# Kernel optimization log

Hardware: AMD Instinct MI355X
Metric: run time of the kernel (lower is better)

The kernel has to match this reference:

```python
import jax, jax.numpy as jnp
import numpy as np

# Dimensions
B_, L_, D_ = 2, 1024, 1024
EXPAND, N_STATE, K_CONV = 2, 16, 4
D_INNER = D_ * EXPAND          # 2048
DT_RANK = (D_ + 15) // 16      # 64 (mamba default: ceil(d_model/16))


def setup_inputs() -> dict:
    key = jax.random.key(0)
    ks = jax.random.split(key, 10)
    sc = 0.02
    x = jax.random.normal(ks[0], (B_, L_, D_), jnp.float32)
    ln_w = jnp.ones((D_,), jnp.float32)
    ln_b = jnp.zeros((D_,), jnp.float32)
    W_in = jax.random.normal(ks[1], (2 * D_INNER, D_), jnp.float32) * sc
    W_conv = jax.random.normal(ks[2], (D_INNER, K_CONV), jnp.float32) * 0.2
    b_conv = jnp.zeros((D_INNER,), jnp.float32)
    W_xproj = jax.random.normal(ks[3], (DT_RANK + 2 * N_STATE, D_INNER), jnp.float32) * sc
    W_dt = jax.random.normal(ks[4], (D_INNER, DT_RANK), jnp.float32) * (DT_RANK ** -0.5)
    # dt bias: inverse softplus of dt ~ U[1e-3, 1e-1] (mamba init)
    dt = jnp.exp(jax.random.uniform(ks[5], (D_INNER,), jnp.float32)
                 * (np.log(0.1) - np.log(0.001)) + np.log(0.001))
    b_dt = dt + jnp.log(-jnp.expm1(-dt))
    # A_log init: log(1..N) per channel (S4D-real init)
    A_log = jnp.log(jnp.broadcast_to(jnp.arange(1, N_STATE + 1, dtype=jnp.float32),
                                     (D_INNER, N_STATE)))
    D_skip = jnp.ones((D_INNER,), jnp.float32)
    W_out = jax.random.normal(ks[6], (D_, D_INNER), jnp.float32) * sc
    return {"x": x, "ln_w": ln_w, "ln_b": ln_b, "W_in": W_in, "W_conv": W_conv,
            "b_conv": b_conv, "W_xproj": W_xproj, "W_dt": W_dt, "b_dt": b_dt,
            "A_log": A_log, "D_skip": D_skip, "W_out": W_out}


def _layernorm(x, w, b, eps=1e-5):
    mu = jnp.mean(x, axis=-1, keepdims=True)
    var = jnp.mean(jnp.square(x - mu), axis=-1, keepdims=True)
    return (x - mu) * jax.lax.rsqrt(var + eps) * w + b


def reference(x, ln_w, ln_b, W_in, W_conv, b_conv, W_xproj, W_dt, b_dt,
              A_log, D_skip, W_out):
    B, L, D = x.shape
    residual = x
    xn = _layernorm(x, ln_w, ln_b)

    # in_proj -> (x_ssm, z), each (B, L, d_inner)
    xz = jnp.einsum('bld,ed->ble', xn, W_in)
    xs, z = jnp.split(xz, 2, axis=-1)

    # causal depthwise conv1d along L + SiLU
    xp = jnp.pad(xs, ((0, 0), (K_CONV - 1, 0), (0, 0)))
    xc = b_conv + sum(xp[:, k:k + L, :] * W_conv[:, k] for k in range(K_CONV))
    xc = jax.nn.silu(xc)

    # input-dependent dt, B, C
    dbl = jnp.einsum('ble,re->blr', xc, W_xproj)
    dt_low = dbl[..., :DT_RANK]
    B_ssm = dbl[..., DT_RANK:DT_RANK + N_STATE]        # (B, L, N)
    C_ssm = dbl[..., DT_RANK + N_STATE:]               # (B, L, N)
    delta = jax.nn.softplus(jnp.einsum('blr,er->ble', dt_low, W_dt) + b_dt)  # (B, L, d_inner)

    A = -jnp.exp(A_log)                                # (d_inner, N)
    dA = jnp.exp(delta[..., None] * A)                 # (B, L, d_inner, N)
    dBx = delta[..., None] * B_ssm[:, :, None, :] * xc[..., None]  # (B, L, d_inner, N)

    def step(h, inp):
        dA_t, dBx_t, C_t = inp
        h = dA_t * h + dBx_t                           # (B, d_inner, N)
        y_t = jnp.einsum('bdn,bn->bd', h, C_t)
        return h, y_t

    h0 = jnp.zeros((B, D_INNER, N_STATE), x.dtype)
    _, ys = jax.lax.scan(step, h0,
                         (dA.transpose(1, 0, 2, 3), dBx.transpose(1, 0, 2, 3),
                          C_ssm.transpose(1, 0, 2)))
    y = ys.transpose(1, 0, 2) + D_skip * xc            # (B, L, d_inner)
    y = y * jax.nn.silu(z)
    out = jnp.einsum('ble,de->bld', y, W_out)
    # dropout is identity in eval mode
    return out + residual
```

## Files before the change

kernel.cpp:

```cpp
#include <hip/hip_runtime.h>
#include <math.h>

#define B_ 2
#define L_ 1024
#define D_ 1024
#define D_INNER 2048
#define DT_RANK 64
#define N_STATE 16
#define NC 32
#define LC 32

typedef __attribute__((ext_vector_type(8))) short bf16x8;
typedef __attribute__((ext_vector_type(4))) float f32x4;

__device__ __forceinline__ unsigned short f2bf(float f) {
  unsigned int u = __float_as_uint(f);
  u += 0x7fffu + ((u >> 16) & 1u);
  return (unsigned short)(u >> 16);
}
__device__ __forceinline__ float bf2f(unsigned short s) {
  return __uint_as_float((unsigned int)s << 16);
}
__device__ __forceinline__ float softplus_f(float v) {
  return (v > 20.0f) ? v : log1pf(__expf(v));
}

__global__ __launch_bounds__(256) void ln_kernel(const float* __restrict__ x,
                                                 const float* __restrict__ w,
                                                 const float* __restrict__ b,
                                                 unsigned short* __restrict__ out) {
  int row = blockIdx.x;
  int tid = threadIdx.x;
  const float* xr = x + (size_t)row * D_;
  float4 v = ((const float4*)xr)[tid];
  float s  = v.x + v.y + v.z + v.w;
  float s2 = v.x*v.x + v.y*v.y + v.z*v.z + v.w*v.w;
  #pragma unroll
  for (int off = 32; off > 0; off >>= 1) {
    s  += __shfl_down(s, off);
    s2 += __shfl_down(s2, off);
  }
  __shared__ float ss[4], ss2[4];
  int wid = tid >> 6, lane = tid & 63;
  if (lane == 0) { ss[wid] = s; ss2[wid] = s2; }
  __syncthreads();
  if (tid == 0) {
    float a  = ss[0] + ss[1] + ss[2] + ss[3];
    float a2 = ss2[0] + ss2[1] + ss2[2] + ss2[3];
    ss[0]  = a  * (1.0f / D_);
    ss2[0] = a2 * (1.0f / D_);
  }
  __syncthreads();
  float mu = ss[0];
  float var = ss2[0] - mu * mu;
  float rstd = rsqrtf(var + 1e-5f);
  float4 wv = ((const float4*)w)[tid];
  float4 bv = ((const float4*)b)[tid];
  ushort4 o;
  o.x = f2bf((v.x - mu) * rstd * wv.x + bv.x);
  o.y = f2bf((v.y - mu) * rstd * wv.y + bv.y);
  o.z = f2bf((v.z - mu) * rstd * wv.z + bv.z);
  o.w = f2bf((v.w - mu) * rstd * wv.w + bv.w);
  ((ushort4*)(out + (size_t)row * D_))[tid] = o;
}

__global__ __launch_bounds__(256) void cvt_bf16_kernel(const float* __restrict__ in,
                                                       unsigned short* __restrict__ out,
                                                       int n4) {
  int i = blockIdx.x * 256 + threadIdx.x;
  if (i >= n4) return;
  float4 v = ((const float4*)in)[i];
  ushort4 o; o.x = f2bf(v.x); o.y = f2bf(v.y); o.z = f2bf(v.z); o.w = f2bf(v.w);
  ((ushort4*)out)[i] = o;
}

__global__ __launch_bounds__(256) void cvt_wxp_kernel(const float* __restrict__ in,
                                                      unsigned short* __restrict__ out) {
  int i = blockIdx.x * 256 + threadIdx.x;
  int row = (i * 4) >> 11;
  ushort4 o = make_ushort4(0, 0, 0, 0);
  if (row < 96) {
    float4 v = ((const float4*)in)[i];
    o.x = f2bf(v.x); o.y = f2bf(v.y); o.z = f2bf(v.z); o.w = f2bf(v.w);
  }
  ((ushort4*)out)[i] = o;
}

template<int EPI, int BMT>
__global__ __launch_bounds__(256) void gemm_mfma(const unsigned short* __restrict__ A, int lda,
                                                 const unsigned short* __restrict__ B, int ldb,
                                                 float* __restrict__ Cf,
                                                 unsigned short* __restrict__ Cb,
                                                 int ldc, int Nguard, int K,
                                                 const float* __restrict__ ep0,
                                                 size_t zstride = 0) {
  __shared__ unsigned short As[BMT * 64];
  __shared__ unsigned short Bs[128 * 64];
  const int tid = threadIdx.x;
  const int lane = tid & 63;
  const int w = tid >> 6;
  const int wr = w >> 1, wc = w & 1;
  const int bm = blockIdx.y * BMT;
  const int bn = blockIdx.x * 128;
  const int l16 = lane & 15;
  constexpr int MW = BMT / 32;

  int kbeg = 0, kend = K;
  if (EPI == 4) {
    int ks = K >> 4;
    kbeg = blockIdx.z * ks;
    kend = kbeg + ks;
    Cf += (size_t)blockIdx.z * zstride;
  }

  f32x4 acc[MW][4];
  #pragma unroll
  for (int m = 0; m < MW; ++m)
    #pragma unroll
    for (int n = 0; n < 4; ++n) acc[m][n] = (f32x4){0.f, 0.f, 0.f, 0.f};

  for (int k0 = kbeg; k0 < kend; k0 += 64) {
    #pragma unroll
    for (int i = 0; i < BMT / 32; ++i) {
      int p = (i * 256 + tid) * 16;
      int r = p >> 7;
      int s = (p >> 4) & 7;
      int cb = ((s ^ (r & 7)) << 3);
      const unsigned short* ga = A + (size_t)(bm + r) * lda + k0 + cb;
      __builtin_amdgcn_global_load_lds(
          (const __attribute__((address_space(1))) void*)ga,
          (__attribute__((address_space(3))) void*)(As + (p >> 1)), 16, 0, 0);
    }
    #pragma unroll
    for (int i = 0; i < 4; ++i) {
      int p = (i * 256 + tid) * 16;
      int r = p >> 7;
      int s = (p >> 4) & 7;
      int cb = ((s ^ (r & 7)) << 3);
      const unsigned short* gb = B + (size_t)(bn + r) * ldb + k0 + cb;
      __builtin_amdgcn_global_load_lds(
          (const __attribute__((address_space(1))) void*)gb,
          (__attribute__((address_space(3))) void*)(Bs + (p >> 1)), 16, 0, 0);
    }
    __syncthreads();
    #pragma unroll
    for (int ks = 0; ks < 2; ++ks) {
      const int slot = ks * 4 + (lane >> 4);
      bf16x8 af[MW], bfr[4];
      #pragma unroll
      for (int m = 0; m < MW; ++m) {
        int ar = wr * (BMT / 2) + m * 16 + l16;
        af[m] = *(const bf16x8*)(As + ar * 64 + ((slot ^ (ar & 7)) << 3));
      }
      #pragma unroll
      for (int n = 0; n < 4; ++n) {
        int br = wc * 64 + n * 16 + l16;
        bfr[n] = *(const bf16x8*)(Bs + br * 64 + ((slot ^ (br & 7)) << 3));
      }
      #pragma unroll
      for (int m = 0; m < MW; ++m)
        #pragma unroll
        for (int n = 0; n < 4; ++n)
          acc[m][n] = __builtin_amdgcn_mfma_f32_16x16x32_bf16(af[m], bfr[n], acc[m][n], 0, 0, 0);
    }
    __syncthreads();
  }

  const int crow0 = bm + wr * (BMT / 2) + (lane >> 4) * 4;
  const int ccol0 = bn + wc * 64 + l16;
  #pragma unroll
  for (int m = 0; m < MW; ++m) {
    #pragma unroll
    for (int n = 0; n < 4; ++n) {
      int c = ccol0 + n * 16;
      if (c >= Nguard) continue;
      #pragma unroll
      for (int r = 0; r < 4; ++r) {
        int rr = crow0 + m * 16 + r;
        float v = acc[m][n][r];
        if (EPI == 2) {
          Cf[(size_t)rr * ldc + c] = v + ep0[(size_t)rr * ldc + c];
        } else if (EPI == 3) {
          if (c < D_INNER) Cf[(size_t)rr * D_INNER + c] = v;
          else             Cb[(size_t)rr * D_INNER + (c - D_INNER)] = f2bf(v);
        } else if (EPI == 5) {
          Cf[(size_t)rr * ldc + c] = softplus_f(v + ep0[c]);
        } else {
          Cf[(size_t)rr * ldc + c] = v;
        }
      }
    }
  }
}

__global__ __launch_bounds__(256) void reduce_dbl_kernel(const float* __restrict__ part,
                                                         float* __restrict__ dblb,
                                                         unsigned short* __restrict__ dtlow_b) {
  int i = blockIdx.x * 256 + threadIdx.x;
  float4 a = ((const float4*)part)[i];
  #pragma unroll
  for (int s = 1; s < 16; ++s) {
    float4 b = ((const float4*)part)[s * 49152 + i];
    a.x += b.x; a.y += b.y; a.z += b.z; a.w += b.w;
  }
  ((float4*)dblb)[i] = a;
  int flat = i * 4;
  int row = flat / 96;
  int col = flat - row * 96;
  if (col < 64) {
    ushort4 o; o.x = f2bf(a.x); o.y = f2bf(a.y); o.z = f2bf(a.z); o.w = f2bf(a.w);
    *(ushort4*)(dtlow_b + (size_t)row * 64 + col) = o;
  }
}

__global__ __launch_bounds__(256) void conv_silu_kernel(const float* __restrict__ xs,
                                                        const float* __restrict__ Wc,
                                                        const float* __restrict__ bc,
                                                        float* __restrict__ xc,
                                                        unsigned short* __restrict__ xcb) {
  int idx = blockIdx.x * 256 + threadIdx.x;
  int e = idx & (D_INNER - 1);
  int t = (idx >> 11) & (L_ - 1);
  float acc = bc[e];
  float w0 = Wc[e * 4 + 0], w1 = Wc[e * 4 + 1], w2 = Wc[e * 4 + 2], w3 = Wc[e * 4 + 3];
  const float* base = xs + (size_t)idx;
  if (t >= 3) acc = fmaf(base[-3 * D_INNER], w0, acc);
  if (t >= 2) acc = fmaf(base[-2 * D_INNER], w1, acc);
  if (t >= 1) acc = fmaf(base[-1 * D_INNER], w2, acc);
  acc = fmaf(base[0], w3, acc);
  float s = acc / (1.0f + __expf(-acc));
  xc[idx] = s;
  xcb[idx] = f2bf(s);
}

__global__ __launch_bounds__(256) void scan1_kernel(const float* __restrict__ delta,
                                                    const float* __restrict__ xc,
                                                    const float* __restrict__ dbl,
                                                    const float* __restrict__ A_log,
                                                    float* __restrict__ P,
                                                    float* __restrict__ Q) {
  int e = blockIdx.x * 256 + threadIdx.x;
  int b = blockIdx.y, c = blockIdx.z;
  const int t0 = (int)(b * L_ + c * LC);

  __shared__ float sB[LC][N_STATE];
  for (int i = threadIdx.x; i < LC * N_STATE; i += 256) {
    int step = i >> 4, n = i & 15;
    sB[step][n] = dbl[(size_t)(t0 + step) * 96 + 64 + n];
  }
  __syncthreads();

  float An[N_STATE];
  #pragma unroll
  for (int q = 0; q < 4; ++q) {
    float4 v = *(const float4*)&A_log[(size_t)e * N_STATE + q * 4];
    An[q*4+0] = -__expf(v.x); An[q*4+1] = -__expf(v.y);
    An[q*4+2] = -__expf(v.z); An[q*4+3] = -__expf(v.w);
  }
  float h[N_STATE], p[N_STATE];
  #pragma unroll
  for (int n = 0; n < N_STATE; ++n) { h[n] = 0.f; p[n] = 1.f; }

  const size_t row0 = (size_t)t0 * D_INNER + e;
  float dlt = delta[row0];
  float xcv = xc[row0];

  for (int tt = 0; tt < LC; ++tt) {
    float ndlt = 0.f, nxcv = 0.f;
    if (tt + 1 < LC) {
      ndlt = delta[row0 + (size_t)(tt + 1) * D_INNER];
      nxcv = xc[row0 + (size_t)(tt + 1) * D_INNER];
    }
    float dbx = dlt * xcv;
    #pragma unroll
    for (int n = 0; n < N_STATE; ++n) {
      float da = __expf(dlt * An[n]);
      h[n] = fmaf(da, h[n], dbx * sB[tt][n]);
      p[n] *= da;
    }
    dlt = ndlt; xcv = nxcv;
  }
  size_t o = ((size_t)(c * B_ + b) * N_STATE) * D_INNER + e;
  #pragma unroll
  for (int n = 0; n < N_STATE; ++n) {
    P[o + (size_t)n * D_INNER] = p[n];
    Q[o + (size_t)n * D_INNER] = h[n];
  }
}

__global__ __launch_bounds__(256) void scan2_kernel(const float* __restrict__ P,
                                                    float* __restrict__ Q) {
  int idx = blockIdx.x * 256 + threadIdx.x;
  float H = 0.f;
  #pragma unroll
  for (int c = 0; c < NC; ++c) {
    size_t o = (size_t)c * (B_ * N_STATE * D_INNER) + idx;
    float p = P[o], q = Q[o];
    Q[o] = H;
    H = fmaf(p, H, q);
  }
}

__global__ __launch_bounds__(256) void scan3_kernel(const float* __restrict__ delta,
                                                    const float* __restrict__ xc,
                                                    const float* __restrict__ dbl,
                                                    const float* __restrict__ A_log,
                                                    const float* __restrict__ Hinit,
                                                    const unsigned short* __restrict__ zb,
                                                    const float* __restrict__ Dsk,
                                                    unsigned short* __restrict__ y) {
  int e = blockIdx.x * 256 + threadIdx.x;
  int b = blockIdx.y, c = blockIdx.z;
  const int t0 = (int)(b * L_ + c * LC);

  __shared__ float sB[LC][N_STATE];
  __shared__ float sC[LC][N_STATE];
  for (int i = threadIdx.x; i < LC * N_STATE; i += 256) {
    int step = i >> 4, n = i & 15;
    const float* row = dbl + (size_t)(t0 + step) * 96;
    sB[step][n] = row[64 + n];
    sC[step][n] = row[80 + n];
  }
  __syncthreads();

  float An[N_STATE];
  #pragma unroll
  for (int q = 0; q < 4; ++q) {
    float4 v = *(const float4*)&A_log[(size_t)e * N_STATE + q * 4];
    An[q*4+0] = -__expf(v.x); An[q*4+1] = -__expf(v.y);
    An[q*4+2] = -__expf(v.z); An[q*4+3] = -__expf(v.w);
  }
  float h[N_STATE];
  {
    size_t o = (size_t)c * (B_ * N_STATE * D_INNER) + (size_t)b * (N_STATE * D_INNER) + e;
    #pragma unroll
    for (int n = 0; n < N_STATE; ++n) h[n] = Hinit[o + (size_t)n * D_INNER];
  }
  float dskip = Dsk[e];
  const size_t row0 = (size_t)t0 * D_INNER + e;

  float dlt = delta[row0];
  float xcv = xc[row0];
  float zv  = bf2f(zb[row0]);

  for (int tt = 0; tt < LC; ++tt) {
    float ndlt = 0.f, nxcv = 0.f, nzv = 0.f;
    if (tt + 1 < LC) {
      ndlt = delta[row0 + (size_t)(tt + 1) * D_INNER];
      nxcv = xc[row0 + (size_t)(tt + 1) * D_INNER];
      nzv  = bf2f(zb[row0 + (size_t)(tt + 1) * D_INNER]);
    }
    float dbx = dlt * xcv;
    float yv = 0.f;
    #pragma unroll
    for (int n = 0; n < N_STATE; ++n) {
      float da = __expf(dlt * An[n]);
      h[n] = fmaf(da, h[n], dbx * sB[tt][n]);
      yv = fmaf(h[n], sC[tt][n], yv);
    }
    float gate = zv / (1.0f + __expf(-zv));
    y[row0 + (size_t)tt * D_INNER] = f2bf((yv + dskip * xcv) * gate);
    dlt = ndlt; xcv = nxcv; zv = nzv;
  }
}

extern "C" void kernel_launch(void* const* d_in, const int* in_sizes, int n_in,
                              void* d_out, int out_size, void* d_ws, size_t ws_size,
                              hipStream_t stream) {
  const float* x       = (const float*)d_in[0];
  const float* ln_w    = (const float*)d_in[1];
  const float* ln_b    = (const float*)d_in[2];
  const float* W_in    = (const float*)d_in[3];
  const float* W_conv  = (const float*)d_in[4];
  const float* b_conv  = (const float*)d_in[5];
  const float* W_xproj = (const float*)d_in[6];
  const float* W_dt    = (const float*)d_in[7];
  const float* b_dt    = (const float*)d_in[8];
  const float* A_log   = (const float*)d_in[9];
  const float* D_skip  = (const float*)d_in[10];
  const float* W_out   = (const float*)d_in[11];
  float* out = (float*)d_out;
  float* ws  = (float*)d_ws;

  const size_t BL = (size_t)B_ * L_;
  float* xs    = ws;
  float* xc    = xs    + BL * D_INNER;
  float* delta = xc    + BL * D_INNER;
  float* dblb  = delta + BL * D_INNER;
  unsigned short* xn_b   = (unsigned short*)(dblb + BL * 96);
  unsigned short* Win_b  = xn_b   + 2097152;
  unsigned short* z_b    = Win_b  + 4194304;
  unsigned short* xc_b   = z_b    + 4194304;
  unsigned short* Wxp_b  = xc_b   + 4194304;
  unsigned short* y_b    = Wxp_b  + 262144;
  unsigned short* Wout_b = y_b    + 4194304;
  unsigned short* dtlow_b= Wout_b + 2097152;
  unsigned short* Wdt_b  = dtlow_b+ 131072;
  float* P    = (float*)xn_b;
  float* Q    = (float*)xc_b;
  float* part = (float*)y_b;

  ln_kernel<<<BL, 256, 0, stream>>>(x, ln_w, ln_b, xn_b);
  cvt_bf16_kernel<<<4096, 256, 0, stream>>>(W_in, Win_b, 1048576);
  cvt_wxp_kernel<<<256, 256, 0, stream>>>(W_xproj, Wxp_b);
  cvt_bf16_kernel<<<128, 256, 0, stream>>>(W_dt, Wdt_b, 32768);
  gemm_mfma<3, 128><<<dim3(32, 16), 256, 0, stream>>>(
      xn_b, D_, Win_b, D_, xs, z_b, D_INNER, 4096, D_, nullptr, 0);
  conv_silu_kernel<<<(BL * D_INNER) / 256, 256, 0, stream>>>(xs, W_conv, b_conv, xc, xc_b);
  gemm_mfma<4, 128><<<dim3(1, 16, 16), 256, 0, stream>>>(
      xc_b, D_INNER, Wxp_b, D_INNER, part, nullptr, 96, 96, D_INNER, nullptr,
      (size_t)2048 * 96);
  reduce_dbl_kernel<<<192, 256, 0, stream>>>(part, dblb, dtlow_b);
  cvt_bf16_kernel<<<2048, 256, 0, stream>>>(W_out, Wout_b, 524288);
  gemm_mfma<5, 128><<<dim3(16, 16), 256, 0, stream>>>(
      dtlow_b, DT_RANK, Wdt_b, DT_RANK, delta, nullptr, D_INNER, D_INNER, DT_RANK, b_dt, 0);
  scan1_kernel<<<dim3(D_INNER / 256, B_, NC), 256, 0, stream>>>(delta, xc, dblb, A_log, P, Q);
  scan2_kernel<<<(B_ * N_STATE * D_INNER) / 256, 256, 0, stream>>>(P, Q);
  scan3_kernel<<<dim3(D_INNER / 256, B_, NC), 256, 0, stream>>>(delta, xc, dblb, A_log, Q,
                                                                z_b, D_skip, y_b);
  gemm_mfma<2, 64><<<dim3(8, 32), 256, 0, stream>>>(
      y_b, D_INNER, Wout_b, D_INNER, out, nullptr, D_, D_, D_INNER, x, 0);
}
```

Measured before the change: 267.4 us.

## Store intermediates in bf16, merge weight conversions, and halve scan chunk length

Stores the in_proj output, delta and the conv output only in bf16, which drops the fp32 copies of xs, xc and delta and cuts memory traffic in the conv and scan kernels. The three weight-conversion kernels become one launch. The scan chunk length changes from 32 to 16, with twice as many chunks, for more parallelism in scan1 and scan3. Workspace now holds separate P and Q buffers. The cost is lower precision in delta and xc during the scan, plus a larger scan2 combine stage.

Result: faster. 260.2 us (-2.7%).

```diff
diff --git a/kernel.cpp b/kernel.cpp
--- a/kernel.cpp
+++ b/kernel.cpp
@@ -7,8 +7,8 @@
 #define D_INNER 2048
 #define DT_RANK 64
 #define N_STATE 16
-#define NC 32
-#define LC 32
+#define NC 64
+#define LC 16
 
 typedef __attribute__((ext_vector_type(8))) short bf16x8;
 typedef __attribute__((ext_vector_type(4))) float f32x4;
@@ -64,26 +64,49 @@
   ((ushort4*)(out + (size_t)row * D_))[tid] = o;
 }
 
-__global__ __launch_bounds__(256) void cvt_bf16_kernel(const float* __restrict__ in,
-                                                       unsigned short* __restrict__ out,
-                                                       int n4) {
+#define N4_WIN  1048576
+#define N4_WOUT  524288
+#define N4_WDT    32768
+#define N4_WXP    65536
+__global__ __launch_bounds__(256) void cvt_all_kernel(const float* __restrict__ W_in,
+                                                      const float* __restrict__ W_out,
+                                                      const float* __restrict__ W_dt,
+                                                      const float* __restrict__ W_xp,
+                                                      unsigned short* __restrict__ Win_b,
+                                                      unsigned short* __restrict__ Wout_b,
+                                                      unsigned short* __restrict__ Wdt_b,
+                                                      unsigned short* __restrict__ Wxp_b) {
   int i = blockIdx.x * 256 + threadIdx.x;
-  if (i >= n4) return;
-  float4 v = ((const float4*)in)[i];
-  ushort4 o; o.x = f2bf(v.x); o.y = f2bf(v.y); o.z = f2bf(v.z); o.w = f2bf(v.w);
-  ((ushort4*)out)[i] = o;
-}
-
-__global__ __launch_bounds__(256) void cvt_wxp_kernel(const float* __restrict__ in,
-                                                      unsigned short* __restrict__ out) {
-  int i = blockIdx.x * 256 + threadIdx.x;
-  int row = (i * 4) >> 11;
-  ushort4 o = make_ushort4(0, 0, 0, 0);
-  if (row < 96) {
-    float4 v = ((const float4*)in)[i];
-    o.x = f2bf(v.x); o.y = f2bf(v.y); o.z = f2bf(v.z); o.w = f2bf(v.w);
-  }
-  ((ushort4*)out)[i] = o;
+  if (i < N4_WIN) {
+    float4 v = ((const float4*)W_in)[i];
+    ushort4 o; o.x = f2bf(v.x); o.y = f2bf(v.y); o.z = f2bf(v.z); o.w = f2bf(v.w);
+    ((ushort4*)Win_b)[i] = o;
+    return;
+  }
+  i -= N4_WIN;
+  if (i < N4_WOUT) {
+    float4 v = ((const float4*)W_out)[i];
+    ushort4 o; o.x = f2bf(v.x); o.y = f2bf(v.y); o.z = f2bf(v.z); o.w = f2bf(v.w);
+    ((ushort4*)Wout_b)[i] = o;
+    return;
+  }
+  i -= N4_WOUT;
+  if (i < N4_WDT) {
+    float4 v = ((const float4*)W_dt)[i];
+    ushort4 o; o.x = f2bf(v.x); o.y = f2bf(v.y); o.z = f2bf(v.z); o.w = f2bf(v.w);
+    ((ushort4*)Wdt_b)[i] = o;
+    return;
+  }
+  i -= N4_WDT;
+  if (i < N4_WXP) {
+    int row = (i * 4) >> 11;
+    ushort4 o = make_ushort4(0, 0, 0, 0);
+    if (row < 96) {
+      float4 v = ((const float4*)W_xp)[i];
+      o.x = f2bf(v.x); o.y = f2bf(v.y); o.z = f2bf(v.z); o.w = f2bf(v.w);
+    }
+    ((ushort4*)Wxp_b)[i] = o;
+  }
 }
 
 template<int EPI, int BMT>
@@ -178,13 +201,12 @@
       for (int r = 0; r < 4; ++r) {
         int rr = crow0 + m * 16 + r;
         float v = acc[m][n][r];
-        if (EPI == 2) {
+        if (EPI == 1) {
+          Cb[(size_t)rr * ldc + c] = f2bf(v);
+        } else if (EPI == 2) {
           Cf[(size_t)rr * ldc + c] = v + ep0[(size_t)rr * ldc + c];
-        } else if (EPI == 3) {
-          if (c < D_INNER) Cf[(size_t)rr * D_INNER + c] = v;
-          else             Cb[(size_t)rr * D_INNER + (c - D_INNER)] = f2bf(v);
         } else if (EPI == 5) {
-          Cf[(size_t)rr * ldc + c] = softplus_f(v + ep0[c]);
+          Cb[(size_t)rr * ldc + c] = f2bf(softplus_f(v + ep0[c]));
         } else {
           Cf[(size_t)rr * ldc + c] = v;
         }
@@ -213,28 +235,27 @@
   }
 }
 
-__global__ __launch_bounds__(256) void conv_silu_kernel(const float* __restrict__ xs,
+__global__ __launch_bounds__(256) void conv_silu_kernel(const unsigned short* __restrict__ xz,
                                                         const float* __restrict__ Wc,
                                                         const float* __restrict__ bc,
-                                                        float* __restrict__ xc,
                                                         unsigned short* __restrict__ xcb) {
   int idx = blockIdx.x * 256 + threadIdx.x;
   int e = idx & (D_INNER - 1);
   int t = (idx >> 11) & (L_ - 1);
+  int bt = idx >> 11;
   float acc = bc[e];
   float w0 = Wc[e * 4 + 0], w1 = Wc[e * 4 + 1], w2 = Wc[e * 4 + 2], w3 = Wc[e * 4 + 3];
-  const float* base = xs + (size_t)idx;
-  if (t >= 3) acc = fmaf(base[-3 * D_INNER], w0, acc);
-  if (t >= 2) acc = fmaf(base[-2 * D_INNER], w1, acc);
-  if (t >= 1) acc = fmaf(base[-1 * D_INNER], w2, acc);
-  acc = fmaf(base[0], w3, acc);
+  const unsigned short* base = xz + (size_t)bt * 4096 + e;
+  if (t >= 3) acc = fmaf(bf2f(base[-3 * 4096]), w0, acc);
+  if (t >= 2) acc = fmaf(bf2f(base[-2 * 4096]), w1, acc);
+  if (t >= 1) acc = fmaf(bf2f(base[-1 * 4096]), w2, acc);
+  acc = fmaf(bf2f(base[0]), w3, acc);
   float s = acc / (1.0f + __expf(-acc));
-  xc[idx] = s;
   xcb[idx] = f2bf(s);
 }
 
-__global__ __launch_bounds__(256) void scan1_kernel(const float* __restrict__ delta,
-                                                    const float* __restrict__ xc,
+__global__ __launch_bounds__(256) void scan1_kernel(const unsigned short* __restrict__ delta,
+                                                    const unsigned short* __restrict__ xc,
                                                     const float* __restrict__ dbl,
                                                     const float* __restrict__ A_log,
                                                     float* __restrict__ P,
@@ -244,8 +265,8 @@
   const int t0 = (int)(b * L_ + c * LC);
 
   __shared__ float sB[LC][N_STATE];
-  for (int i = threadIdx.x; i < LC * N_STATE; i += 256) {
-    int step = i >> 4, n = i & 15;
+  {
+    int step = threadIdx.x >> 4, n = threadIdx.x & 15;
     sB[step][n] = dbl[(size_t)(t0 + step) * 96 + 64 + n];
   }
   __syncthreads();
@@ -262,14 +283,14 @@
   for (int n = 0; n < N_STATE; ++n) { h[n] = 0.f; p[n] = 1.f; }
 
   const size_t row0 = (size_t)t0 * D_INNER + e;
-  float dlt = delta[row0];
-  float xcv = xc[row0];
+  float dlt = bf2f(delta[row0]);
+  float xcv = bf2f(xc[row0]);
 
   for (int tt = 0; tt < LC; ++tt) {
     float ndlt = 0.f, nxcv = 0.f;
     if (tt + 1 < LC) {
-      ndlt = delta[row0 + (size_t)(tt + 1) * D_INNER];
-      nxcv = xc[row0 + (size_t)(tt + 1) * D_INNER];
+      ndlt = bf2f(delta[row0 + (size_t)(tt + 1) * D_INNER]);
+      nxcv = bf2f(xc[row0 + (size_t)(tt + 1) * D_INNER]);
     }
     float dbx = dlt * xcv;
     #pragma unroll
@@ -301,12 +322,12 @@
   }
 }
 
-__global__ __launch_bounds__(256) void scan3_kernel(const float* __restrict__ delta,
-                                                    const float* __restrict__ xc,
+__global__ __launch_bounds__(256) void scan3_kernel(const unsigned short* __restrict__ delta,
+                                                    const unsigned short* __restrict__ xc,
                                                     const float* __restrict__ dbl,
                                                     const float* __restrict__ A_log,
                                                     const float* __restrict__ Hinit,
-                                                    const unsigned short* __restrict__ zb,
+                                                    const unsigned short* __restrict__ xz,
                                                     const float* __restrict__ Dsk,
                                                     unsigned short* __restrict__ y) {
   int e = blockIdx.x * 256 + threadIdx.x;
@@ -315,8 +336,8 @@
 
   __shared__ float sB[LC][N_STATE];
   __shared__ float sC[LC][N_STATE];
-  for (int i = threadIdx.x; i < LC * N_STATE; i += 256) {
-    int step = i >> 4, n = i & 15;
+  {
+    int step = threadIdx.x >> 4, n = threadIdx.x & 15;
     const float* row = dbl + (size_t)(t0 + step) * 96;
     sB[step][n] = row[64 + n];
     sC[step][n] = row[80 + n];
@@ -332,23 +353,24 @@
   }
   float h[N_STATE];
   {
-    size_t o = (size_t)c * (B_ * N_STATE * D_INNER) + (size_t)b * (N_STATE * D_INNER) + e;
+    size_t o = ((size_t)(c * B_ + b) * N_STATE) * D_INNER + e;
     #pragma unroll
     for (int n = 0; n < N_STATE; ++n) h[n] = Hinit[o + (size_t)n * D_INNER];
   }
   float dskip = Dsk[e];
   const size_t row0 = (size_t)t0 * D_INNER + e;
-
-  float dlt = delta[row0];
-  float xcv = xc[row0];
-  float zv  = bf2f(zb[row0]);
+  const size_t zrow0 = (size_t)t0 * 4096 + D_INNER + e;
+
+  float dlt = bf2f(delta[row0]);
+  float xcv = bf2f(xc[row0]);
+  float zv  = bf2f(xz[zrow0]);
 
   for (int tt = 0; tt < LC; ++tt) {
     float ndlt = 0.f, nxcv = 0.f, nzv = 0.f;
     if (tt + 1 < LC) {
-      ndlt = delta[row0 + (size_t)(tt + 1) * D_INNER];
-      nxcv = xc[row0 + (size_t)(tt + 1) * D_INNER];
-      nzv  = bf2f(zb[row0 + (size_t)(tt + 1) * D_INNER]);
+      ndlt = bf2f(delta[row0 + (size_t)(tt + 1) * D_INNER]);
+      nxcv = bf2f(xc[row0 + (size_t)(tt + 1) * D_INNER]);
+      nzv  = bf2f(xz[zrow0 + (size_t)(tt + 1) * 4096]);
     }
     float dbx = dlt * xcv;
     float yv = 0.f;
@@ -380,44 +402,39 @@
   const float* D_skip  = (const float*)d_in[10];
   const float* W_out   = (const float*)d_in[11];
   float* out = (float*)d_out;
-  float* ws  = (float*)d_ws;
 
   const size_t BL = (size_t)B_ * L_;
-  float* xs    = ws;
-  float* xc    = xs    + BL * D_INNER;
-  float* delta = xc    + BL * D_INNER;
-  float* dblb  = delta + BL * D_INNER;
-  unsigned short* xn_b   = (unsigned short*)(dblb + BL * 96);
-  unsigned short* Win_b  = xn_b   + 2097152;
-  unsigned short* z_b    = Win_b  + 4194304;
-  unsigned short* xc_b   = z_b    + 4194304;
-  unsigned short* Wxp_b  = xc_b   + 4194304;
-  unsigned short* y_b    = Wxp_b  + 262144;
-  unsigned short* Wout_b = y_b    + 4194304;
-  unsigned short* dtlow_b= Wout_b + 2097152;
-  unsigned short* Wdt_b  = dtlow_b+ 131072;
-  float* P    = (float*)xn_b;
-  float* Q    = (float*)xc_b;
-  float* part = (float*)y_b;
+  float* dblb = (float*)d_ws;
+  float* part = dblb + 196608;
+  float* P    = part + 3145728;
+  float* Q    = P    + 4194304;
+  unsigned short* xn_b    = (unsigned short*)(Q + 4194304);
+  unsigned short* Win_b   = xn_b    + 2097152;
+  unsigned short* xz_b    = Win_b   + 4194304;
+  unsigned short* xc_b    = xz_b    + 8388608;
+  unsigned short* Wxp_b   = xc_b    + 4194304;
+  unsigned short* y_b     = Wxp_b   + 262144;
+  unsigned short* Wout_b  = y_b     + 4194304;
+  unsigned short* dtlow_b = Wout_b  + 2097152;
+  unsigned short* Wdt_b   = dtlow_b + 131072;
+  unsigned short* delta_b = Wdt_b   + 131072;
 
   ln_kernel<<<BL, 256, 0, stream>>>(x, ln_w, ln_b, xn_b);
-  cvt_bf16_kernel<<<4096, 256, 0, stream>>>(W_in, Win_b, 1048576);
-  cvt_wxp_kernel<<<256, 256, 0, stream>>>(W_xproj, Wxp_b);
-  cvt_bf16_kernel<<<128, 256, 0, stream>>>(W_dt, Wdt_b, 32768);
-  gemm_mfma<3, 128><<<dim3(32, 16), 256, 0, stream>>>(
-      xn_b, D_, Win_b, D_, xs, z_b, D_INNER, 4096, D_, nullptr, 0);
-  conv_silu_kernel<<<(BL * D_INNER) / 256, 256, 0, stream>>>(xs, W_conv, b_conv, xc, xc_b);
+  cvt_all_kernel<<<(N4_WIN + N4_WOUT + N4_WDT + N4_WXP + 255) / 256, 256, 0, stream>>>(
+      W_in, W_out, W_dt, W_xproj, Win_b, Wout_b, Wdt_b, Wxp_b);
+  gemm_mfma<1, 128><<<dim3(32, 16), 256, 0, stream>>>(
+      xn_b, D_, Win_b, D_, nullptr, xz_b, 4096, 4096, D_, nullptr, 0);
+  conv_silu_kernel<<<(BL * D_INNER) / 256, 256, 0, stream>>>(xz_b, W_conv, b_conv, xc_b);
   gemm_mfma<4, 128><<<dim3(1, 16, 16), 256, 0, stream>>>(
       xc_b, D_INNER, Wxp_b, D_INNER, part, nullptr, 96, 96, D_INNER, nullptr,
       (size_t)2048 * 96);
   reduce_dbl_kernel<<<192, 256, 0, stream>>>(part, dblb, dtlow_b);
-  cvt_bf16_kernel<<<2048, 256, 0, stream>>>(W_out, Wout_b, 524288);
   gemm_mfma<5, 128><<<dim3(16, 16), 256, 0, stream>>>(
-      dtlow_b, DT_RANK, Wdt_b, DT_RANK, delta, nullptr, D_INNER, D_INNER, DT_RANK, b_dt, 0);
-  scan1_kernel<<<dim3(D_INNER / 256, B_, NC), 256, 0, stream>>>(delta, xc, dblb, A_log, P, Q);
+      dtlow_b, DT_RANK, Wdt_b, DT_RANK, nullptr, delta_b, D_INNER, D_INNER, DT_RANK, b_dt, 0);
+  scan1_kernel<<<dim3(D_INNER / 256, B_, NC), 256, 0, stream>>>(delta_b, xc_b, dblb, A_log, P, Q);
   scan2_kernel<<<(B_ * N_STATE * D_INNER) / 256, 256, 0, stream>>>(P, Q);
-  scan3_kernel<<<dim3(D_INNER / 256, B_, NC), 256, 0, stream>>>(delta, xc, dblb, A_log, Q,
-                                                                z_b, D_skip, y_b);
+  scan3_kernel<<<dim3(D_INNER / 256, B_, NC), 256, 0, stream>>>(delta_b, xc_b, dblb, A_log, Q,
+                                                                xz_b, D_skip, y_b);
   gemm_mfma<2, 64><<<dim3(8, 32), 256, 0, stream>>>(
       y_b, D_INNER, Wout_b, D_INNER, out, nullptr, D_, D_, D_INNER, x, 0);
 }
```
